# Performance work log

Measured on AMD Instinct MI355X. Metric: run time of the kernel, lower is better.

## Reference

```python
import jax, jax.numpy as jnp
import numpy as np

N_NODES = 100000
N_EDGES = 1600000
IN_DIM = 128
OUT_DIM = 32


def setup_inputs() -> dict:
    key = jax.random.key(0)
    k1, k2, k3, k4, k5 = jax.random.split(key, 5)
    x = jax.random.normal(k1, (N_NODES, IN_DIM), dtype=jnp.float32)
    adj_rows = jax.random.randint(k2, (N_EDGES,), 0, N_NODES, dtype=jnp.int32)
    adj_cols = jax.random.randint(k3, (N_EDGES,), 0, N_NODES, dtype=jnp.int32)
    adj_vals = jax.random.uniform(k4, (N_EDGES,), dtype=jnp.float32)
    # kaiming-uniform-like init for weight, zeros for bias (as in init_parameters)
    bound = float(np.sqrt(6.0 / IN_DIM))
    weight = jax.random.uniform(k5, (IN_DIM, OUT_DIM), minval=-bound, maxval=bound, dtype=jnp.float32)
    bias = jnp.zeros((OUT_DIM,), dtype=jnp.float32)
    return {"x": x, "adj_rows": adj_rows, "adj_cols": adj_cols,
            "adj_vals": adj_vals, "weight": weight, "bias": bias}


def reference(x, adj_rows, adj_cols, adj_vals, weight, bias):
    # support = X @ W  -> [N, OUT_DIM]
    support = x @ weight
    # output = A_sparse @ support  (COO SpMM via gather + segment-sum)
    gathered = adj_vals[:, None] * support[adj_cols]          # [E, OUT_DIM]
    output = jax.ops.segment_sum(gathered, adj_rows, num_segments=N_NODES)
    return output + bias
```

## Files before the change

kernel.cpp:

```cpp
#include <hip/hip_runtime.h>

#define N_NODES 100000
#define N_EDGES 1600000
#define IN_DIM 128
#define OUT_DIM 32

typedef _Float16 h2 __attribute__((ext_vector_type(2)));

__global__ __launch_bounds__(256) void gemm_support(
    const float* __restrict__ x, const float* __restrict__ w,
    float* __restrict__ support) {
  __shared__ float ws[IN_DIM][OUT_DIM];
  __shared__ float xs[8][IN_DIM];
  const int tid = threadIdx.x;

  for (int i = tid; i < IN_DIM * OUT_DIM; i += 256)
    ws[i / OUT_DIM][i % OUT_DIM] = w[i];

  const int row0 = blockIdx.x * 8;
  for (int i = tid; i < 8 * IN_DIM; i += 256) {
    const int r = i / IN_DIM, k = i % IN_DIM;
    const int row = row0 + r;
    xs[r][k] = (row < N_NODES) ? x[(long long)row * IN_DIM + k] : 0.f;
  }
  __syncthreads();

  const int r = tid >> 5;
  const int c = tid & 31;
  const int row = row0 + r;
  if (row >= N_NODES) return;

  float acc = 0.f;
#pragma unroll
  for (int k = 0; k < IN_DIM; ++k)
    acc = fmaf(xs[r][k], ws[k][c], acc);
  support[(long long)row * OUT_DIM + c] = acc;
}

__device__ __forceinline__ void pk_atomic_add_h2(h2* p, h2 v) {
#if __has_builtin(__builtin_amdgcn_global_atomic_fadd_v2f16)
  __builtin_amdgcn_global_atomic_fadd_v2f16(
      (__attribute__((address_space(1))) h2*)p, v);
#else
  unsigned* pu = (unsigned*)p;
  unsigned old = *pu;
  while (true) {
    h2 cur = __builtin_bit_cast(h2, old);
    h2 nv = cur + v;
    unsigned n = __builtin_bit_cast(unsigned, nv);
    unsigned r = atomicCAS(pu, old, n);
    if (r == old) break;
    old = r;
  }
#endif
}

__global__ __launch_bounds__(256) void scatter_h2(
    const int* __restrict__ rows, const int* __restrict__ cols,
    const float* __restrict__ vals, const float* __restrict__ support,
    h2* __restrict__ out_h) {
  const long long gid = (long long)blockIdx.x * 256 + threadIdx.x;
  if (gid >= (long long)N_EDGES * 16) return;
  const int e = (int)(gid >> 4);
  const int l = (int)(gid & 15);
  const int r = rows[e];
  const int c = cols[e];
  const float v = vals[e];
  const float2 s = *(const float2*)(support + (long long)c * OUT_DIM + 2 * l);
  h2 inc = { (_Float16)(v * s.x), (_Float16)(v * s.y) };
  pk_atomic_add_h2(out_h + (long long)r * 16 + l, inc);
}

__global__ __launch_bounds__(256) void finalize_h(
    const h2* __restrict__ out_h, const float* __restrict__ bias,
    float* __restrict__ out) {
  const int i = blockIdx.x * 256 + threadIdx.x;
  if (i >= N_NODES * OUT_DIM / 8) return;
  const h2* src = out_h + i * 4;
  float4 a, b;
  h2 p0 = src[0], p1 = src[1], p2 = src[2], p3 = src[3];
  const int d0 = (i * 8) & 31;
  a.x = (float)p0[0] + bias[d0 + 0];
  a.y = (float)p0[1] + bias[d0 + 1];
  a.z = (float)p1[0] + bias[d0 + 2];
  a.w = (float)p1[1] + bias[d0 + 3];
  b.x = (float)p2[0] + bias[d0 + 4];
  b.y = (float)p2[1] + bias[d0 + 5];
  b.z = (float)p3[0] + bias[d0 + 6];
  b.w = (float)p3[1] + bias[d0 + 7];
  float4* dst = (float4*)(out + (long long)i * 8);
  dst[0] = a;
  dst[1] = b;
}

extern "C" void kernel_launch(void* const* d_in, const int* in_sizes, int n_in,
                              void* d_out, int out_size, void* d_ws, size_t ws_size,
                              hipStream_t stream) {
  const float* x        = (const float*)d_in[0];
  const int*   adj_rows = (const int*)d_in[1];
  const int*   adj_cols = (const int*)d_in[2];
  const float* adj_vals = (const float*)d_in[3];
  const float* weight   = (const float*)d_in[4];
  const float* bias     = (const float*)d_in[5];
  float* out = (float*)d_out;

  char* wsp = (char*)d_ws;
  float* support = (float*)wsp;
  h2* out_h = (h2*)(wsp + 12800000);

  hipMemsetAsync(out_h, 0, (size_t)N_NODES * OUT_DIM * sizeof(_Float16),
                 stream);
  gemm_support<<<(N_NODES + 7) / 8, 256, 0, stream>>>(x, weight, support);

  {
    const long long total = (long long)N_EDGES * 16;
    scatter_h2<<<(int)((total + 255) / 256), 256, 0, stream>>>(
        adj_rows, adj_cols, adj_vals, support, out_h);
  }
  {
    const int total = N_NODES * OUT_DIM / 8;
    finalize_h<<<(total + 255) / 256, 256, 0, stream>>>(out_h, bias, out);
  }
}
```

Before: 147.3 us.

## Store support in fp16, fuse output zeroing into GEMM, vectorize loads

The support matrix is now written in half precision, which halves its footprint and the bytes each edge gathers in the scatter kernel. The separate memset of the fp16 accumulator is removed and folded into the GEMM kernel, saving one launch. The GEMM's shared-memory loads now use float4 and drop bounds checks, relying on N_NODES being a multiple of 8. The extra fp16 rounding of support adds a little error before accumulation.

```diff
diff --git a/kernel.cpp b/kernel.cpp
--- a/kernel.cpp
+++ b/kernel.cpp
@@ -9,32 +9,34 @@
 
 __global__ __launch_bounds__(256) void gemm_support(
     const float* __restrict__ x, const float* __restrict__ w,
-    float* __restrict__ support) {
+    _Float16* __restrict__ support, unsigned* __restrict__ out_h_words) {
   __shared__ float ws[IN_DIM][OUT_DIM];
   __shared__ float xs[8][IN_DIM];
   const int tid = threadIdx.x;
 
-  for (int i = tid; i < IN_DIM * OUT_DIM; i += 256)
-    ws[i / OUT_DIM][i % OUT_DIM] = w[i];
-
+  {
+    const float4* w4 = (const float4*)w;
+    float4* ws4 = (float4*)&ws[0][0];
+    for (int i = tid; i < IN_DIM * OUT_DIM / 4; i += 256) ws4[i] = w4[i];
+  }
   const int row0 = blockIdx.x * 8;
-  for (int i = tid; i < 8 * IN_DIM; i += 256) {
-    const int r = i / IN_DIM, k = i % IN_DIM;
-    const int row = row0 + r;
-    xs[r][k] = (row < N_NODES) ? x[(long long)row * IN_DIM + k] : 0.f;
+  {
+    const float4* x4 = (const float4*)(x + (long long)row0 * IN_DIM);
+    float4* xs4 = (float4*)&xs[0][0];
+    xs4[tid] = x4[tid];
   }
   __syncthreads();
 
   const int r = tid >> 5;
   const int c = tid & 31;
-  const int row = row0 + r;
-  if (row >= N_NODES) return;
-
   float acc = 0.f;
 #pragma unroll
   for (int k = 0; k < IN_DIM; ++k)
     acc = fmaf(xs[r][k], ws[k][c], acc);
-  support[(long long)row * OUT_DIM + c] = acc;
+  support[(long long)(row0 + r) * OUT_DIM + c] = (_Float16)acc;
+
+  const int g = blockIdx.x * 256 + tid;
+  if (g < N_NODES * OUT_DIM / 2) out_h_words[g] = 0u;
 }
 
 __device__ __forceinline__ void pk_atomic_add_h2(h2* p, h2 v) {
@@ -57,7 +59,7 @@
 
 __global__ __launch_bounds__(256) void scatter_h2(
     const int* __restrict__ rows, const int* __restrict__ cols,
-    const float* __restrict__ vals, const float* __restrict__ support,
+    const float* __restrict__ vals, const _Float16* __restrict__ support,
     h2* __restrict__ out_h) {
   const long long gid = (long long)blockIdx.x * 256 + threadIdx.x;
   if (gid >= (long long)N_EDGES * 16) return;
@@ -66,8 +68,8 @@
   const int r = rows[e];
   const int c = cols[e];
   const float v = vals[e];
-  const float2 s = *(const float2*)(support + (long long)c * OUT_DIM + 2 * l);
-  h2 inc = { (_Float16)(v * s.x), (_Float16)(v * s.y) };
+  const h2 s = *(const h2*)(support + (long long)c * OUT_DIM + 2 * l);
+  h2 inc = { (_Float16)(v * (float)s[0]), (_Float16)(v * (float)s[1]) };
   pk_atomic_add_h2(out_h + (long long)r * 16 + l, inc);
 }
 
@@ -105,13 +107,11 @@
   float* out = (float*)d_out;
 
   char* wsp = (char*)d_ws;
-  float* support = (float*)wsp;
-  h2* out_h = (h2*)(wsp + 12800000);
+  _Float16* support = (_Float16*)wsp;
+  h2* out_h = (h2*)(wsp + 6400000);
 
-  hipMemsetAsync(out_h, 0, (size_t)N_NODES * OUT_DIM * sizeof(_Float16),
-                 stream);
-  gemm_support<<<(N_NODES + 7) / 8, 256, 0, stream>>>(x, weight, support);
-
+  gemm_support<<<N_NODES / 8, 256, 0, stream>>>(x, weight, support,
+                                                (unsigned*)out_h);
   {
     const long long total = (long long)N_EDGES * 16;
     scatter_h2<<<(int)((total + 255) / 256), 256, 0, stream>>>(
```

After: 134.1 us. 9.0% less time.
